# Kernel optimization log

Measured on AMD Instinct MI355X. Metric: run time of the kernel, lower is better.

Reference implementation:

```python
import jax, jax.numpy as jnp
import numpy as np

IMG = 128
FX, FY, CX, CY = 588.03, 587.07, 320.0, 240.0
FLIP = 1.0
SAMPLE = 1024  # sample_num in Img2pcl
N_VERTS = 778


def setup_inputs() -> dict:
    key = jax.random.key(0)
    ks = jax.random.split(key, 6)
    B = 64
    real = jax.random.uniform(ks[0], (B, 1, IMG, IMG), jnp.float32)   # normalized depth in [0,1)
    synth = jax.random.uniform(ks[1], (B, 1, IMG, IMG), jnp.float32)  # unused by forward
    verts = jax.random.normal(ks[2], (B, N_VERTS, 3), jnp.float32)
    faces = jax.random.randint(ks[3], (1538, 3), 0, N_VERTS, jnp.int32)  # unused by forward
    center = jax.random.normal(ks[4], (B, 3), jnp.float32) * 0.1 + jnp.array([0.0, 0.0, 400.0], jnp.float32)
    # crop matrix must be invertible: identity plus small perturbation
    M = jnp.eye(3, dtype=jnp.float32)[None] + 0.1 * jax.random.normal(ks[5], (B, 3, 3), jnp.float32)
    cube = jnp.full((B, 3), 250.0, jnp.float32)
    return dict(real=real, synth=synth, verts=verts, faces=faces, center=center, M=M, cube=cube)


def _img2pcl(real, center, M, cube):
    """Vectorized Img2pcl: normalized (u,v,d) -> normalized xyz for every pixel, plus valid mask."""
    B = real.shape[0]
    # input already IMG x IMG so F.interpolate is identity
    img = real[:, 0]                                   # [B,H,W]
    t = 2.0 * jnp.arange(IMG, dtype=jnp.float32) / (IMG - 1.0) - 1.0
    mesh_x = jnp.broadcast_to(t[:, None], (IMG, IMG))  # varies along rows (v)
    mesh_y = jnp.broadcast_to(t[None, :], (IMG, IMG))  # varies along cols (u)
    uvd = jnp.stack([
        jnp.broadcast_to(mesh_y, (B, IMG, IMG)),
        jnp.broadcast_to(mesh_x, (B, IMG, IMG)),
        img,
    ], axis=-1).reshape(B, IMG * IMG, 3)               # [B,P,3]
    # unnormalize uv and depth
    uv = (uvd[..., :2] + 1.0) * (IMG / 2.0)
    d = uvd[..., 2] * (cube[:, None, 2] / 2.0) + center[:, None, 2]   # [B,P]
    # get_trans_points with M^{-1}
    M_inv = jnp.linalg.inv(M)                          # [B,3,3]
    h = jnp.concatenate([uv, jnp.ones_like(uv[..., :1])], axis=-1)    # [B,P,3]
    uv_w = jnp.einsum('bij,bpj->bpi', M_inv, h)[..., :2]
    # pointsImgTo3D (pinhole back-projection)
    x = (uv_w[..., 0] - CX) * d / FX
    y = FLIP * (uv_w[..., 1] - CY) * d / FY
    xyz = jnp.stack([x, y, d], axis=-1)                # [B,P,3]
    xyz_n = (xyz - center[:, None, :]) / (cube[:, None, :] / 2.0)
    mask = img.reshape(B, -1) <= 0.99                  # valid (foreground) pixels
    return xyz_n, mask


def reference(real, synth, verts, faces, center, M, cube):
    xyz, mask = _img2pcl(real, center, M, cube)
    # torch.multinomial(uniform weights, SAMPLE, without replacement) over valid pixels
    # == Gumbel top-k over the masked candidate set (jit-compatible, fixed shapes)
    u = jax.random.uniform(jax.random.key(1), mask.shape)
    gumbel = -jnp.log(-jnp.log(u + 1e-20) + 1e-20)
    score = jnp.where(mask, gumbel, -jnp.inf)
    _, idx = jax.lax.top_k(score, SAMPLE)              # [B,SAMPLE]
    pcl1 = jnp.take_along_axis(xyz, idx[..., None], axis=1)  # [B,SAMPLE,3]
    # chamfer distance (pytorch3d-style: mean-reduced squared-dist NN, both directions)
    d2 = jnp.sum((pcl1[:, :, None, :] - verts[:, None, :, :]) ** 2, axis=-1)  # [B,SAMPLE,V]
    loss = d2.min(axis=2).mean() + d2.min(axis=1).mean()
    return loss
```

## Files before the change

### kernel.cpp

```cpp
#include <hip/hip_runtime.h>
#include <stdint.h>
#include <math.h>

#define NPIX   16384
#define SAMPLE 1024
#define NV     778
#define BATCH  64

#define A_SCALE (1.0f / (float)(BATCH * SAMPLE))
#define B_SCALE (1.0f / (float)(BATCH * NV))

__device__ __forceinline__ uint32_t rotl32(uint32_t v, int r) {
  return (v << r) | (v >> (32 - r));
}

__device__ __forceinline__ uint32_t threefry_bits(uint32_t g) {
  uint32_t ks0 = 0u, ks1 = 1u;
  uint32_t ks2 = ks0 ^ ks1 ^ 0x1BD11BDAu;
  uint32_t x0 = 0u + ks0, x1 = g + ks1;
#define TF_R(r) { x0 += x1; x1 = rotl32(x1, (r)); x1 ^= x0; }
  TF_R(13) TF_R(15) TF_R(26) TF_R(6)
  x0 += ks1; x1 += ks2 + 1u;
  TF_R(17) TF_R(29) TF_R(16) TF_R(24)
  x0 += ks2; x1 += ks0 + 2u;
  TF_R(13) TF_R(15) TF_R(26) TF_R(6)
  x0 += ks0; x1 += ks1 + 3u;
  TF_R(17) TF_R(29) TF_R(16) TF_R(24)
  x0 += ks1; x1 += ks2 + 4u;
  TF_R(13) TF_R(15) TF_R(26) TF_R(6)
  x0 += ks2; x1 += ks0 + 5u;
#undef TF_R
  return x0 ^ x1;
}

__device__ __forceinline__ float waveReduceSum(float v) {
#pragma unroll
  for (int off = 32; off > 0; off >>= 1) v += __shfl_down(v, off, 64);
  return v;
}

__global__ __launch_bounds__(1024) void select_kernel(
    const float4* __restrict__ real4,
    const float* __restrict__ center,
    const float* __restrict__ M,
    const float* __restrict__ cube,
    float4* __restrict__ pcl4,
    float* __restrict__ out) {
  const int b = blockIdx.x;
  const int tid = threadIdx.x;
  const int lane = tid & 63;
  const int wv = tid >> 6;

  if (b == 0 && tid == 0) out[0] = 0.0f;

  __shared__ uint32_t hist[512];
  __shared__ uint32_t wt[8], offs[8];
  __shared__ uint64_t cand[512];
  __shared__ float candrv[512];
  __shared__ float sh_minv[6], sh_c[3], sh_hb[3];
  __shared__ uint32_t sh_cnt, sh_ccnt, sh_bstar, sh_above;

  if (tid == 0) {
    const float* m = M + (size_t)b * 9;
    float m00=m[0], m01=m[1], m02=m[2];
    float m10=m[3], m11=m[4], m12=m[5];
    float m20=m[6], m21=m[7], m22=m[8];
    float c00 = m11*m22 - m12*m21;
    float c10 = m12*m20 - m10*m22;
    float c20 = m10*m21 - m11*m20;
    float det = m00*c00 + m01*c10 + m02*c20;
    float id = 1.0f / det;
    sh_minv[0] = c00 * id;
    sh_minv[1] = (m02*m21 - m01*m22) * id;
    sh_minv[2] = (m01*m12 - m02*m11) * id;
    sh_minv[3] = c10 * id;
    sh_minv[4] = (m00*m22 - m02*m20) * id;
    sh_minv[5] = (m02*m10 - m00*m12) * id;
    sh_c[0] = center[b*3+0]; sh_c[1] = center[b*3+1]; sh_c[2] = center[b*3+2];
    sh_hb[0] = cube[b*3+0]*0.5f; sh_hb[1] = cube[b*3+1]*0.5f; sh_hb[2] = cube[b*3+2]*0.5f;
    sh_cnt = 0; sh_ccnt = 0;
  }
  if (tid < 512) hist[tid] = 0;

  uint32_t uv[16];
  float    rv[16];
  const float4* rb4 = real4 + (size_t)b * (NPIX / 4);
#pragma unroll
  for (int e4 = 0; e4 < 4; ++e4) {
    float4 im = rb4[e4 * 1024 + tid];
    uint32_t base = (uint32_t)(b * NPIX + e4 * 4096) + (uint32_t)(tid << 2);
    rv[e4*4+0] = im.x; rv[e4*4+1] = im.y; rv[e4*4+2] = im.z; rv[e4*4+3] = im.w;
    uv[e4*4+0] = (im.x <= 0.99f) ? ((threefry_bits(base + 0u) >> 9) + 1u) : 0u;
    uv[e4*4+1] = (im.y <= 0.99f) ? ((threefry_bits(base + 1u) >> 9) + 1u) : 0u;
    uv[e4*4+2] = (im.z <= 0.99f) ? ((threefry_bits(base + 2u) >> 9) + 1u) : 0u;
    uv[e4*4+3] = (im.w <= 0.99f) ? ((threefry_bits(base + 3u) >> 9) + 1u) : 0u;
  }
  __syncthreads();

#pragma unroll
  for (int e = 0; e < 16; ++e)
    if (uv[e]) atomicAdd(&hist[(uv[e] - 1u) >> 14], 1u);
  __syncthreads();

  uint32_t cnt = 0, sfx = 0;
  if (tid < 512) {
    cnt = hist[tid];
    sfx = cnt;
#pragma unroll
    for (int off = 1; off < 64; off <<= 1) {
      uint32_t u = __shfl_down(sfx, off, 64);
      if (lane + off < 64) sfx += u;
    }
    if (lane == 0) wt[wv] = sfx;
  }
  __syncthreads();
  if (tid < 8) {
    uint32_t t = wt[tid], s = t;
#pragma unroll
    for (int off = 1; off < 8; off <<= 1) {
      uint32_t u = __shfl_down(s, off, 64);
      if (tid + off < 8) s += u;
    }
    offs[tid] = s - t;
  }
  __syncthreads();
  if (tid < 512) {
    uint32_t tot = sfx + offs[wv];
    uint32_t above = tot - cnt;
    if (tot >= SAMPLE && above < SAMPLE && cnt > 0) {
      sh_bstar = (uint32_t)tid;
      sh_above = above;
    }
  }
  __syncthreads();
  const int bstar = (int)sh_bstar;
  const uint32_t kneed = SAMPLE - sh_above;

  float4* ob = pcl4 + (size_t)b * SAMPLE;
  auto emit = [&](int p, float depth01, uint32_t slot) {
    int i = p >> 7, j = p & 127;
    float tj = (2.0f * (float)j) / 127.0f - 1.0f;
    float ti = (2.0f * (float)i) / 127.0f - 1.0f;
    float u0 = (tj + 1.0f) * 64.0f;
    float u1 = (ti + 1.0f) * 64.0f;
    float d  = depth01 * sh_hb[2] + sh_c[2];
    float w0 = sh_minv[0]*u0 + sh_minv[1]*u1 + sh_minv[2];
    float w1 = sh_minv[3]*u0 + sh_minv[4]*u1 + sh_minv[5];
    float x = (w0 - 320.0f) * d / 588.03f;
    float y = (w1 - 240.0f) * d / 587.07f;
    float4 o;
    o.x = (x - sh_c[0]) / sh_hb[0];
    o.y = (y - sh_c[1]) / sh_hb[1];
    o.z = (d - sh_c[2]) / sh_hb[2];
    o.w = 0.0f;
    ob[slot] = o;
  };

#pragma unroll
  for (int e = 0; e < 16; ++e) {
    uint32_t v = uv[e];
    int p = (e >> 2) * 4096 + (tid << 2) + (e & 3);
    int bk = v ? (int)((v - 1u) >> 14) : -1;
    bool hi = (bk > bstar);
    unsigned long long m = __ballot(hi);
    if (m) {
      int leader = __ffsll((unsigned long long)m) - 1;
      uint32_t base;
      if (lane == leader) base = atomicAdd(&sh_cnt, (uint32_t)__popcll(m));
      base = __shfl(base, leader, 64);
      if (hi) emit(p, rv[e], base + (uint32_t)__popcll(m & ((1ull << lane) - 1ull)));
    }
    bool eqb = (bk == bstar);
    unsigned long long m2 = __ballot(eqb);
    if (m2) {
      int leader = __ffsll((unsigned long long)m2) - 1;
      uint32_t cb;
      if (lane == leader) cb = atomicAdd(&sh_ccnt, (uint32_t)__popcll(m2));
      cb = __shfl(cb, leader, 64);
      if (eqb) {
        uint32_t ci = cb + (uint32_t)__popcll(m2 & ((1ull << lane) - 1ull));
        if (ci < 512) {
          cand[ci] = ((uint64_t)v << 14) | (uint64_t)(16383 - p);
          candrv[ci] = rv[e];
        }
      }
    }
  }
  __syncthreads();

  uint32_t c = sh_ccnt; if (c > 512) c = 512;
  if (tid < 64) {
    for (uint32_t basei = 0; basei < c; basei += 64) {
      uint32_t i = basei + (uint32_t)lane;
      bool act = (i < c);
      uint64_t ki = act ? cand[i] : 0ull;
      uint32_t rank = 0;
      for (uint32_t j2 = 0; j2 < c; ++j2) rank += (cand[j2] > ki) ? 1u : 0u;
      bool sel = act && (rank < kneed);
      unsigned long long m = __ballot(sel);
      if (m) {
        int leader = __ffsll((unsigned long long)m) - 1;
        uint32_t base;
        if (lane == leader) base = atomicAdd(&sh_cnt, (uint32_t)__popcll(m));
        base = __shfl(base, leader, 64);
        if (sel) {
          int p = 16383 - (int)(ki & 0x3FFFull);
          emit(p, candrv[i], base + (uint32_t)__popcll(m & ((1ull << lane) - 1ull)));
        }
      }
    }
  }
}

#define NA_BLOCKS 512
#define NB_SLICES 7
#define NB_BLOCKS (BATCH * NB_SLICES)

__global__ __launch_bounds__(256, 4) void dist_kernel(
    const float* __restrict__ verts,
    const float4* __restrict__ pcl4,
    float* __restrict__ out) {
  __shared__ __align__(16) uint8_t shbuf[20992];
  __shared__ float red[4];
  const int blk = blockIdx.x;
  const int tid = threadIdx.x;
  const int s = tid >> 5;
  const int g = tid & 31;
  float val = 0.0f;

  if (blk < NA_BLOCKS) {
    const int b = blk >> 3, slice = blk & 7;
    float4* sv4 = (float4*)shbuf;
    float* pmin = (float*)(shbuf + 12448);
    float* npl  = (float*)(shbuf + 16544);
    const float* vb = verts + (size_t)b * NV * 3;
    for (int v = tid; v < NV; v += 256) {
      float x = vb[v*3], y = vb[v*3+1], z = vb[v*3+2];
      float4 t;
      t.x = -2.0f*x; t.y = -2.0f*y; t.z = -2.0f*z; t.w = x*x + y*y + z*z;
      sv4[v] = t;
    }
    const float4* pb = pcl4 + (size_t)b * SAMPLE + slice * 128;
    float px[4], py[4], pz[4], np[4], mn[4];
#pragma unroll
    for (int j = 0; j < 4; ++j) {
      float4 q = pb[j * 32 + g];
      px[j] = q.x; py[j] = q.y; pz[j] = q.z;
      np[j] = q.x*q.x + q.y*q.y + q.z*q.z;
      mn[j] = INFINITY;
    }
    __syncthreads();
    const int vs = s * 98;
    const int ve = (vs + 98 < NV) ? vs + 98 : NV;
    for (int v = vs; v < ve; ++v) {
      float4 vv = sv4[v];
#pragma unroll
      for (int j = 0; j < 4; ++j) {
        float t = fmaf(pz[j], vv.z, fmaf(py[j], vv.y, fmaf(px[j], vv.x, vv.w)));
        mn[j] = fminf(mn[j], t);
      }
    }
#pragma unroll
    for (int j = 0; j < 4; ++j) {
      pmin[s * 128 + j * 32 + g] = mn[j];
      if (s == 0) npl[j * 32 + g] = np[j];
    }
    __syncthreads();
    if (tid < 128) {
      float m = pmin[tid];
#pragma unroll
      for (int ss = 1; ss < 8; ++ss) m = fminf(m, pmin[ss * 128 + tid]);
      val = (m + npl[tid]) * A_SCALE;
    }
  } else {
    const int bb = blk - NA_BLOCKS;
    const int b = bb / NB_SLICES, slice = bb % NB_SLICES;
    float4* sp4 = (float4*)shbuf;
    float* vmin = (float*)(shbuf + 16384);
    float* nvl  = (float*)(shbuf + 20480);
    const float4* pcb = pcl4 + (size_t)b * SAMPLE;
    for (int i = tid; i < SAMPLE; i += 256) {
      float4 q = pcb[i];
      float4 t;
      t.x = -2.0f*q.x; t.y = -2.0f*q.y; t.z = -2.0f*q.z;
      t.w = q.x*q.x + q.y*q.y + q.z*q.z;
      sp4[i] = t;
    }
    const float* vb = verts + (size_t)b * NV * 3;
    const int vbase = slice * 128;
    float vx[4], vy[4], vz[4], nv[4], mn[4];
#pragma unroll
    for (int j = 0; j < 4; ++j) {
      int v = vbase + j * 32 + g;
      int vc = (v < NV) ? v : 0;
      vx[j] = vb[vc*3]; vy[j] = vb[vc*3+1]; vz[j] = vb[vc*3+2];
      nv[j] = vx[j]*vx[j] + vy[j]*vy[j] + vz[j]*vz[j];
      mn[j] = INFINITY;
    }
    __syncthreads();
    const int ps = s * 128;
    for (int i = 0; i < 128; ++i) {
      float4 pt = sp4[ps + i];
#pragma unroll
      for (int j = 0; j < 4; ++j) {
        float t = fmaf(vz[j], pt.z, fmaf(vy[j], pt.y, fmaf(vx[j], pt.x, pt.w)));
        mn[j] = fminf(mn[j], t);
      }
    }
#pragma unroll
    for (int j = 0; j < 4; ++j) {
      vmin[s * 128 + j * 32 + g] = mn[j];
      if (s == 0) nvl[j * 32 + g] = nv[j];
    }
    __syncthreads();
    if (tid < 128 && (vbase + tid) < NV) {
      float m = vmin[tid];
#pragma unroll
      for (int ss = 1; ss < 8; ++ss) m = fminf(m, vmin[ss * 128 + tid]);
      val = (m + nvl[tid]) * B_SCALE;
    }
  }

  float r = waveReduceSum(val);
  if ((tid & 63) == 0) red[tid >> 6] = r;
  __syncthreads();
  if (tid == 0) atomicAdd(out, red[0] + red[1] + red[2] + red[3]);
}

extern "C" void kernel_launch(void* const* d_in, const int* in_sizes, int n_in,
                              void* d_out, int out_size, void* d_ws, size_t ws_size,
                              hipStream_t stream) {
  const float* real   = (const float*)d_in[0];
  const float* verts  = (const float*)d_in[2];
  const float* center = (const float*)d_in[4];
  const float* M      = (const float*)d_in[5];
  const float* cube   = (const float*)d_in[6];

  float4* pcl4 = (float4*)d_ws;
  float* out = (float*)d_out;

  select_kernel<<<dim3(BATCH), dim3(1024), 0, stream>>>(
      (const float4*)real, center, M, cube, pcl4, out);
  dist_kernel<<<dim3(NA_BLOCKS + NB_BLOCKS), dim3(256), 0, stream>>>(
      verts, pcl4, out);
}
```

Before: 115.8 us.

## Fuse select and chamfer into one cooperative kernel with four blocks per batch

Replaces the two-launch pipeline (select_kernel with 64 blocks, then dist_kernel) with one cooperative kernel of 256 blocks, four per batch item, synchronised by grid.sync. Each block handles a quarter of the pixels for the histogram radix threshold and emit step. Boundary-bucket candidates go through global memory for a rank-based tie resolution, and each block then computes a quarter of the chamfer distances. This aims to use more CUs in the selection phase and to drop a kernel launch, at the cost of three grid-wide barriers, global atomics and a cooperative-launch requirement with fallback to the old path.

After: 252.6 us. 2.18x slower.

```diff
diff --git a/kernel.cpp b/kernel.cpp
--- a/kernel.cpp
+++ b/kernel.cpp
@@ -1,6 +1,9 @@
 #include <hip/hip_runtime.h>
+#include <hip/hip_cooperative_groups.h>
 #include <stdint.h>
 #include <math.h>
+
+namespace cg = cooperative_groups;
 
 #define NPIX   16384
 #define SAMPLE 1024
@@ -9,6 +12,14 @@
 
 #define A_SCALE (1.0f / (float)(BATCH * SAMPLE))
 #define B_SCALE (1.0f / (float)(BATCH * NV))
+
+#define WS_PCL    0u
+#define WS_HISTP  1048576u
+#define WS_CAND   1572864u
+#define WS_CANDRV 1835008u
+#define WS_CNT    1966080u
+#define WS_CCNT   1966336u
+#define WS_NEEDED 1966592u
 
 __device__ __forceinline__ uint32_t rotl32(uint32_t v, int r) {
   return (v << r) | (v >> (32 - r));
@@ -37,6 +48,291 @@
 #pragma unroll
   for (int off = 32; off > 0; off >>= 1) v += __shfl_down(v, off, 64);
   return v;
+}
+
+__global__ __launch_bounds__(1024) void fused_kernel(
+    const float4* __restrict__ real4,
+    const float* __restrict__ verts,
+    const float* __restrict__ center,
+    const float* __restrict__ M,
+    const float* __restrict__ cube,
+    float* __restrict__ out,
+    float4* __restrict__ pcl4,
+    uint32_t* __restrict__ histp,
+    uint64_t* __restrict__ candg,
+    float* __restrict__ candrvg,
+    uint32_t* __restrict__ cnts,
+    uint32_t* __restrict__ ccnts) {
+  cg::grid_group grid = cg::this_grid();
+  const int bq = blockIdx.x;
+  const int b = bq >> 2, q = bq & 3;
+  const int tid = threadIdx.x;
+  const int lane = tid & 63;
+  const int wv = tid >> 6;
+
+  __shared__ __align__(16) uint8_t shbuf[45216];
+  __shared__ uint32_t wt[8], offs[8];
+  __shared__ float sh_minv[6], sh_c[3], sh_hb[3];
+  __shared__ uint32_t sh_bstar, sh_above;
+  __shared__ float red[16];
+
+  uint32_t* hist = (uint32_t*)shbuf;
+
+  if (bq == 0 && tid == 0) out[0] = 0.0f;
+  if (q == 0 && tid == 0) { cnts[b] = 0u; ccnts[b] = 0u; }
+  if (tid == 0) {
+    const float* m = M + (size_t)b * 9;
+    float m00=m[0], m01=m[1], m02=m[2];
+    float m10=m[3], m11=m[4], m12=m[5];
+    float m20=m[6], m21=m[7], m22=m[8];
+    float c00 = m11*m22 - m12*m21;
+    float c10 = m12*m20 - m10*m22;
+    float c20 = m10*m21 - m11*m20;
+    float det = m00*c00 + m01*c10 + m02*c20;
+    float id = 1.0f / det;
+    sh_minv[0] = c00 * id;
+    sh_minv[1] = (m02*m21 - m01*m22) * id;
+    sh_minv[2] = (m01*m12 - m02*m11) * id;
+    sh_minv[3] = c10 * id;
+    sh_minv[4] = (m00*m22 - m02*m20) * id;
+    sh_minv[5] = (m02*m10 - m00*m12) * id;
+    sh_c[0] = center[b*3+0]; sh_c[1] = center[b*3+1]; sh_c[2] = center[b*3+2];
+    sh_hb[0] = cube[b*3+0]*0.5f; sh_hb[1] = cube[b*3+1]*0.5f; sh_hb[2] = cube[b*3+2]*0.5f;
+  }
+  if (tid < 512) hist[tid] = 0u;
+
+  float4 im = real4[(size_t)b * 4096 + q * 1024 + tid];
+  uint32_t base = (uint32_t)(b * NPIX + q * 4096) + (uint32_t)(tid << 2);
+  uint32_t uvr[4]; float rvr[4];
+  rvr[0] = im.x; rvr[1] = im.y; rvr[2] = im.z; rvr[3] = im.w;
+  uvr[0] = (im.x <= 0.99f) ? ((threefry_bits(base + 0u) >> 9) + 1u) : 0u;
+  uvr[1] = (im.y <= 0.99f) ? ((threefry_bits(base + 1u) >> 9) + 1u) : 0u;
+  uvr[2] = (im.z <= 0.99f) ? ((threefry_bits(base + 2u) >> 9) + 1u) : 0u;
+  uvr[3] = (im.w <= 0.99f) ? ((threefry_bits(base + 3u) >> 9) + 1u) : 0u;
+  __syncthreads();
+#pragma unroll
+  for (int c = 0; c < 4; ++c)
+    if (uvr[c]) atomicAdd(&hist[(uvr[c] - 1u) >> 14], 1u);
+  __syncthreads();
+  if (tid < 512) histp[(size_t)bq * 512 + tid] = hist[tid];
+
+  grid.sync();
+
+  uint32_t cnt = 0, sfx = 0;
+  if (tid < 512) {
+    const uint32_t* hp = histp + (size_t)(b << 2) * 512 + tid;
+    cnt = hp[0] + hp[512] + hp[1024] + hp[1536];
+    sfx = cnt;
+#pragma unroll
+    for (int off = 1; off < 64; off <<= 1) {
+      uint32_t u = __shfl_down(sfx, off, 64);
+      if (lane + off < 64) sfx += u;
+    }
+    if (lane == 0) wt[wv] = sfx;
+  }
+  __syncthreads();
+  if (tid < 8) {
+    uint32_t t = wt[tid], s = t;
+#pragma unroll
+    for (int off = 1; off < 8; off <<= 1) {
+      uint32_t u = __shfl_down(s, off, 64);
+      if (tid + off < 8) s += u;
+    }
+    offs[tid] = s - t;
+  }
+  __syncthreads();
+  if (tid < 512) {
+    uint32_t tot = sfx + offs[wv];
+    uint32_t above = tot - cnt;
+    if (tot >= SAMPLE && above < SAMPLE && cnt > 0) {
+      sh_bstar = (uint32_t)tid;
+      sh_above = above;
+    }
+  }
+  __syncthreads();
+  const int bstar = (int)sh_bstar;
+  const uint32_t kneed = SAMPLE - sh_above;
+
+  float4* ob = pcl4 + (size_t)b * SAMPLE;
+  auto emit = [&](int p, float depth01, uint32_t slot) {
+    int i = p >> 7, j = p & 127;
+    float tj = (2.0f * (float)j) / 127.0f - 1.0f;
+    float ti = (2.0f * (float)i) / 127.0f - 1.0f;
+    float u0 = (tj + 1.0f) * 64.0f;
+    float u1 = (ti + 1.0f) * 64.0f;
+    float d  = depth01 * sh_hb[2] + sh_c[2];
+    float w0 = sh_minv[0]*u0 + sh_minv[1]*u1 + sh_minv[2];
+    float w1 = sh_minv[3]*u0 + sh_minv[4]*u1 + sh_minv[5];
+    float x = (w0 - 320.0f) * d / 588.03f;
+    float y = (w1 - 240.0f) * d / 587.07f;
+    float4 o;
+    o.x = (x - sh_c[0]) / sh_hb[0];
+    o.y = (y - sh_c[1]) / sh_hb[1];
+    o.z = (d - sh_c[2]) / sh_hb[2];
+    o.w = 0.0f;
+    ob[slot] = o;
+  };
+
+  uint64_t* cb_ = candg + (size_t)b * 512;
+  float*    crv_ = candrvg + (size_t)b * 512;
+#pragma unroll
+  for (int c = 0; c < 4; ++c) {
+    uint32_t v = uvr[c];
+    int p = q * 4096 + (tid << 2) + c;
+    int bk = v ? (int)((v - 1u) >> 14) : -1;
+    bool hi = (bk > bstar);
+    unsigned long long m = __ballot(hi);
+    if (m) {
+      int leader = __ffsll((unsigned long long)m) - 1;
+      uint32_t bslot;
+      if (lane == leader) bslot = atomicAdd(&cnts[b], (uint32_t)__popcll(m));
+      bslot = __shfl(bslot, leader, 64);
+      if (hi) emit(p, rvr[c], bslot + (uint32_t)__popcll(m & ((1ull << lane) - 1ull)));
+    }
+    bool eqb = (bk == bstar);
+    unsigned long long m2 = __ballot(eqb);
+    if (m2) {
+      int leader = __ffsll((unsigned long long)m2) - 1;
+      uint32_t cb;
+      if (lane == leader) cb = atomicAdd(&ccnts[b], (uint32_t)__popcll(m2));
+      cb = __shfl(cb, leader, 64);
+      if (eqb) {
+        uint32_t ci = cb + (uint32_t)__popcll(m2 & ((1ull << lane) - 1ull));
+        if (ci < 512) {
+          cb_[ci] = ((uint64_t)v << 14) | (uint64_t)(16383 - p);
+          crv_[ci] = rvr[c];
+        }
+      }
+    }
+  }
+
+  grid.sync();
+
+  if (q == 0) {
+    uint32_t c = ccnts[b]; if (c > 512u) c = 512u;
+    if (tid < 64) {
+      for (uint32_t basei = 0; basei < c; basei += 64) {
+        uint32_t i = basei + (uint32_t)lane;
+        bool act = (i < c);
+        uint64_t ki = act ? cb_[i] : 0ull;
+        uint32_t rank = 0;
+        for (uint32_t j2 = 0; j2 < c; ++j2) rank += (cb_[j2] > ki) ? 1u : 0u;
+        bool sel = act && (rank < kneed);
+        unsigned long long m = __ballot(sel);
+        if (m) {
+          int leader = __ffsll((unsigned long long)m) - 1;
+          uint32_t bslot;
+          if (lane == leader) bslot = atomicAdd(&cnts[b], (uint32_t)__popcll(m));
+          bslot = __shfl(bslot, leader, 64);
+          if (sel) {
+            int p = 16383 - (int)(ki & 0x3FFFull);
+            emit(p, crv_[i], bslot + (uint32_t)__popcll(m & ((1ull << lane) - 1ull)));
+          }
+        }
+      }
+    }
+  }
+
+  grid.sync();
+
+  float4* sv4 = (float4*)shbuf;
+  float4* sp4 = (float4*)(shbuf + 12448);
+  float*  fbuf = (float*)(shbuf + 28832);
+
+  const float* vb = verts + (size_t)b * NV * 3;
+  if (tid < NV) {
+    float x = vb[tid*3], y = vb[tid*3+1], z = vb[tid*3+2];
+    float4 t;
+    t.x = -2.0f*x; t.y = -2.0f*y; t.z = -2.0f*z; t.w = x*x + y*y + z*z;
+    sv4[tid] = t;
+  }
+  {
+    float4 qd = ob[tid];
+    float4 t;
+    t.x = -2.0f*qd.x; t.y = -2.0f*qd.y; t.z = -2.0f*qd.z;
+    t.w = qd.x*qd.x + qd.y*qd.y + qd.z*qd.z;
+    sp4[tid] = t;
+  }
+  __syncthreads();
+
+  float val = 0.0f;
+  const int sub = tid & 63;
+  const int seg16 = tid >> 6;
+
+  {
+    float px[4], py[4], pz[4], mnA[4];
+#pragma unroll
+    for (int j = 0; j < 4; ++j) {
+      float4 sp = sp4[q * 256 + j * 64 + sub];
+      px[j] = -0.5f * sp.x; py[j] = -0.5f * sp.y; pz[j] = -0.5f * sp.z;
+      mnA[j] = INFINITY;
+    }
+    int vs = seg16 * 49, ve = vs + 49; if (ve > NV) ve = NV;
+    for (int v = vs; v < ve; ++v) {
+      float4 vv = sv4[v];
+#pragma unroll
+      for (int j = 0; j < 4; ++j) {
+        float t = fmaf(pz[j], vv.z, fmaf(py[j], vv.y, fmaf(px[j], vv.x, vv.w)));
+        mnA[j] = fminf(mnA[j], t);
+      }
+    }
+#pragma unroll
+    for (int j = 0; j < 4; ++j) fbuf[seg16 * 256 + j * 64 + sub] = mnA[j];
+  }
+  __syncthreads();
+  if (tid < 256) {
+    float m = fbuf[tid];
+#pragma unroll
+    for (int s2 = 1; s2 < 16; ++s2) m = fminf(m, fbuf[s2 * 256 + tid]);
+    val += (m + sp4[q * 256 + tid].w) * A_SCALE;
+  }
+  __syncthreads();
+
+  {
+    const int vbase = q * 195;
+    int nsl = NV - vbase; if (nsl > 195) nsl = 195;
+    float vx[4], vy[4], vz[4], mnB[4];
+#pragma unroll
+    for (int j = 0; j < 4; ++j) {
+      int vloc = j * 64 + sub;
+      int vi = (vloc < nsl) ? (vbase + vloc) : 0;
+      float4 sv = sv4[vi];
+      vx[j] = -0.5f * sv.x; vy[j] = -0.5f * sv.y; vz[j] = -0.5f * sv.z;
+      mnB[j] = INFINITY;
+    }
+    int is = seg16 * 64;
+    for (int i = 0; i < 64; ++i) {
+      float4 pp = sp4[is + i];
+#pragma unroll
+      for (int j = 0; j < 4; ++j) {
+        float t = fmaf(vz[j], pp.z, fmaf(vy[j], pp.y, fmaf(vx[j], pp.x, pp.w)));
+        mnB[j] = fminf(mnB[j], t);
+      }
+    }
+#pragma unroll
+    for (int j = 0; j < 4; ++j) fbuf[seg16 * 256 + j * 64 + sub] = mnB[j];
+  }
+  __syncthreads();
+  {
+    const int vbase = q * 195;
+    int nsl = NV - vbase; if (nsl > 195) nsl = 195;
+    if (tid < nsl) {
+      float m = fbuf[tid];
+#pragma unroll
+      for (int s2 = 1; s2 < 16; ++s2) m = fminf(m, fbuf[s2 * 256 + tid]);
+      val += (m + sv4[vbase + tid].w) * B_SCALE;
+    }
+  }
+
+  float r = waveReduceSum(val);
+  if (lane == 0) red[wv] = r;
+  __syncthreads();
+  if (tid == 0) {
+    float s = 0.0f;
+#pragma unroll
+    for (int i = 0; i < 16; ++i) s += red[i];
+    atomicAdd(out, s);
+  }
 }
 
 __global__ __launch_bounds__(1024) void select_kernel(
@@ -335,9 +631,37 @@
   const float* center = (const float*)d_in[4];
   const float* M      = (const float*)d_in[5];
   const float* cube   = (const float*)d_in[6];
-
-  float4* pcl4 = (float4*)d_ws;
   float* out = (float*)d_out;
+
+  uint8_t* w = (uint8_t*)d_ws;
+  float4*   pcl4    = (float4*)(w + WS_PCL);
+  uint32_t* histp   = (uint32_t*)(w + WS_HISTP);
+  uint64_t* candg   = (uint64_t*)(w + WS_CAND);
+  float*    candrvg = (float*)(w + WS_CANDRV);
+  uint32_t* cnts    = (uint32_t*)(w + WS_CNT);
+  uint32_t* ccnts   = (uint32_t*)(w + WS_CCNT);
+
+  static int coop = -1;
+  if (coop < 0) {
+    int dev = 0, v = 0;
+    (void)hipGetDevice(&dev);
+    if (hipDeviceGetAttribute(&v, hipDeviceAttributeCooperativeLaunch, dev) != hipSuccess) v = 0;
+    coop = v ? 1 : 0;
+  }
+
+  if (coop == 1 && ws_size >= (size_t)WS_NEEDED) {
+    const float4* real4 = (const float4*)real;
+    void* args[] = {
+      (void*)&real4, (void*)&verts, (void*)&center, (void*)&M, (void*)&cube,
+      (void*)&out, (void*)&pcl4, (void*)&histp, (void*)&candg, (void*)&candrvg,
+      (void*)&cnts, (void*)&ccnts
+    };
+    hipError_t e = hipLaunchCooperativeKernel(
+        reinterpret_cast<void*>(fused_kernel), dim3(BATCH * 4), dim3(1024),
+        args, 0, stream);
+    if (e == hipSuccess) return;
+    (void)hipGetLastError();
+  }
 
   select_kernel<<<dim3(BATCH), dim3(1024), 0, stream>>>(
       (const float4*)real, center, M, cube, pcl4, out);
```

## Fuse selection and chamfer distance into one kernel with redundant per-quarter selection

Applied to the files above, without the earlier changes.

Merges the sampling/selection kernel and the distance kernel into a single launch of 256 blocks, four per batch. Each block redoes the full top-k selection for its batch and keeps the selected points in shared memory, then computes one quarter of each chamfer direction. Atomic-based compaction is replaced with deterministic block-wide prefix scans, and the output is zeroed with a memset. This removes the global workspace round trip and the second launch, at the cost of repeating the threefry hashing and selection four times per batch and using large shared memory with 1024-thread blocks.

Result: faster. 109.9 us (-5.2%).

```diff
diff --git a/kernel.cpp b/kernel.cpp
--- a/kernel.cpp
+++ b/kernel.cpp
@@ -39,26 +39,60 @@
   return v;
 }
 
-__global__ __launch_bounds__(1024) void select_kernel(
+__device__ __forceinline__ uint32_t blockExclScan1024(
+    uint32_t v, volatile uint32_t* swt, volatile uint32_t* soffs,
+    uint32_t* total) {
+  const int tid = threadIdx.x;
+  const int lane = tid & 63;
+  const int wv = tid >> 6;
+  __syncthreads();
+  uint32_t incl = v;
+#pragma unroll
+  for (int off = 1; off < 64; off <<= 1) {
+    uint32_t u = __shfl_up(incl, off, 64);
+    if (lane >= off) incl += u;
+  }
+  if (lane == 63) swt[wv] = incl;
+  __syncthreads();
+  if (tid < 16) {
+    uint32_t t = swt[tid], s = t;
+#pragma unroll
+    for (int off = 1; off < 16; off <<= 1) {
+      uint32_t u = __shfl_up(s, off, 64);
+      if (lane >= off) s += u;
+    }
+    soffs[tid] = s - t;
+  }
+  __syncthreads();
+  *total = soffs[15] + swt[15];
+  return soffs[wv] + incl - v;
+}
+
+__global__ __launch_bounds__(1024) void mega_kernel(
     const float4* __restrict__ real4,
+    const float* __restrict__ verts,
     const float* __restrict__ center,
     const float* __restrict__ M,
     const float* __restrict__ cube,
-    float4* __restrict__ pcl4,
     float* __restrict__ out) {
-  const int b = blockIdx.x;
+  const int bq = blockIdx.x;
+  const int b = bq >> 2, q = bq & 3;
   const int tid = threadIdx.x;
   const int lane = tid & 63;
   const int wv = tid >> 6;
 
-  if (b == 0 && tid == 0) out[0] = 0.0f;
-
-  __shared__ uint32_t hist[512];
+  __shared__ __align__(16) uint8_t shbuf[53408];
+  float4*   sv4    = (float4*)shbuf;
+  float4*   sp4    = (float4*)(shbuf + 12448);
+  float*    fbuf   = (float*)(shbuf + 28832);
+  uint32_t* hist   = (uint32_t*)(shbuf + 45216);
+  uint64_t* cand   = (uint64_t*)(shbuf + 47264);
+  float*    candrv = (float*)(shbuf + 51360);
   __shared__ uint32_t wt[8], offs[8];
-  __shared__ uint64_t cand[512];
-  __shared__ float candrv[512];
+  __shared__ uint32_t swt[16], soffs[16];
   __shared__ float sh_minv[6], sh_c[3], sh_hb[3];
-  __shared__ uint32_t sh_cnt, sh_ccnt, sh_bstar, sh_above;
+  __shared__ uint32_t sh_bstar, sh_above;
+  __shared__ float red[16];
 
   if (tid == 0) {
     const float* m = M + (size_t)b * 9;
@@ -78,18 +112,25 @@
     sh_minv[5] = (m02*m10 - m00*m12) * id;
     sh_c[0] = center[b*3+0]; sh_c[1] = center[b*3+1]; sh_c[2] = center[b*3+2];
     sh_hb[0] = cube[b*3+0]*0.5f; sh_hb[1] = cube[b*3+1]*0.5f; sh_hb[2] = cube[b*3+2]*0.5f;
-    sh_cnt = 0; sh_ccnt = 0;
-  }
-  if (tid < 512) hist[tid] = 0;
+  }
+  if (tid < 512) hist[tid] = 0u;
+
+  const float* vb = verts + (size_t)b * NV * 3;
+  for (int v = tid; v < NV; v += 1024) {
+    float x = vb[v*3], y = vb[v*3+1], z = vb[v*3+2];
+    float4 t;
+    t.x = -2.0f*x; t.y = -2.0f*y; t.z = -2.0f*z; t.w = x*x + y*y + z*z;
+    sv4[v] = t;
+  }
 
   uint32_t uv[16];
-  float    rv[16];
+  float    rvv[16];
   const float4* rb4 = real4 + (size_t)b * (NPIX / 4);
 #pragma unroll
   for (int e4 = 0; e4 < 4; ++e4) {
     float4 im = rb4[e4 * 1024 + tid];
     uint32_t base = (uint32_t)(b * NPIX + e4 * 4096) + (uint32_t)(tid << 2);
-    rv[e4*4+0] = im.x; rv[e4*4+1] = im.y; rv[e4*4+2] = im.z; rv[e4*4+3] = im.w;
+    rvv[e4*4+0] = im.x; rvv[e4*4+1] = im.y; rvv[e4*4+2] = im.z; rvv[e4*4+3] = im.w;
     uv[e4*4+0] = (im.x <= 0.99f) ? ((threefry_bits(base + 0u) >> 9) + 1u) : 0u;
     uv[e4*4+1] = (im.y <= 0.99f) ? ((threefry_bits(base + 1u) >> 9) + 1u) : 0u;
     uv[e4*4+2] = (im.z <= 0.99f) ? ((threefry_bits(base + 2u) >> 9) + 1u) : 0u;
@@ -134,9 +175,9 @@
   }
   __syncthreads();
   const int bstar = (int)sh_bstar;
-  const uint32_t kneed = SAMPLE - sh_above;
-
-  float4* ob = pcl4 + (size_t)b * SAMPLE;
+  const uint32_t above = sh_above;
+  const uint32_t kneed = SAMPLE - above;
+
   auto emit = [&](int p, float depth01, uint32_t slot) {
     int i = p >> 7, j = p & 127;
     float tj = (2.0f * (float)j) / 127.0f - 1.0f;
@@ -148,183 +189,140 @@
     float w1 = sh_minv[3]*u0 + sh_minv[4]*u1 + sh_minv[5];
     float x = (w0 - 320.0f) * d / 588.03f;
     float y = (w1 - 240.0f) * d / 587.07f;
-    float4 o;
-    o.x = (x - sh_c[0]) / sh_hb[0];
-    o.y = (y - sh_c[1]) / sh_hb[1];
-    o.z = (d - sh_c[2]) / sh_hb[2];
-    o.w = 0.0f;
-    ob[slot] = o;
+    float ox = (x - sh_c[0]) / sh_hb[0];
+    float oy = (y - sh_c[1]) / sh_hb[1];
+    float oz = (d - sh_c[2]) / sh_hb[2];
+    float4 t;
+    t.x = -2.0f*ox; t.y = -2.0f*oy; t.z = -2.0f*oz;
+    t.w = ox*ox + oy*oy + oz*oz;
+    sp4[slot] = t;
   };
 
+  uint32_t ch = 0, ce = 0;
 #pragma unroll
   for (int e = 0; e < 16; ++e) {
-    uint32_t v = uv[e];
-    int p = (e >> 2) * 4096 + (tid << 2) + (e & 3);
-    int bk = v ? (int)((v - 1u) >> 14) : -1;
-    bool hi = (bk > bstar);
-    unsigned long long m = __ballot(hi);
-    if (m) {
-      int leader = __ffsll((unsigned long long)m) - 1;
-      uint32_t base;
-      if (lane == leader) base = atomicAdd(&sh_cnt, (uint32_t)__popcll(m));
-      base = __shfl(base, leader, 64);
-      if (hi) emit(p, rv[e], base + (uint32_t)__popcll(m & ((1ull << lane) - 1ull)));
-    }
-    bool eqb = (bk == bstar);
-    unsigned long long m2 = __ballot(eqb);
-    if (m2) {
-      int leader = __ffsll((unsigned long long)m2) - 1;
-      uint32_t cb;
-      if (lane == leader) cb = atomicAdd(&sh_ccnt, (uint32_t)__popcll(m2));
-      cb = __shfl(cb, leader, 64);
-      if (eqb) {
-        uint32_t ci = cb + (uint32_t)__popcll(m2 & ((1ull << lane) - 1ull));
-        if (ci < 512) {
-          cand[ci] = ((uint64_t)v << 14) | (uint64_t)(16383 - p);
-          candrv[ci] = rv[e];
+    int bk = uv[e] ? (int)((uv[e] - 1u) >> 14) : -1;
+    ch += (bk > bstar) ? 1u : 0u;
+    ce += (bk == bstar) ? 1u : 0u;
+  }
+  uint32_t htot, etot;
+  uint32_t hoff = blockExclScan1024(ch, swt, soffs, &htot);
+  uint32_t eoff = blockExclScan1024(ce, swt, soffs, &etot);
+
+  {
+    uint32_t h = hoff, eo = eoff;
+#pragma unroll
+    for (int e = 0; e < 16; ++e) {
+      uint32_t v = uv[e];
+      int bk = v ? (int)((v - 1u) >> 14) : -1;
+      int p = (e >> 2) * 4096 + (tid << 2) + (e & 3);
+      if (bk > bstar) {
+        emit(p, rvv[e], h++);
+      } else if (bk == bstar) {
+        if (eo < 512u) {
+          cand[eo] = ((uint64_t)v << 14) | (uint64_t)(16383 - p);
+          candrv[eo] = rvv[e];
         }
+        eo++;
       }
     }
   }
   __syncthreads();
 
-  uint32_t c = sh_ccnt; if (c > 512) c = 512;
-  if (tid < 64) {
-    for (uint32_t basei = 0; basei < c; basei += 64) {
-      uint32_t i = basei + (uint32_t)lane;
-      bool act = (i < c);
-      uint64_t ki = act ? cand[i] : 0ull;
-      uint32_t rank = 0;
-      for (uint32_t j2 = 0; j2 < c; ++j2) rank += (cand[j2] > ki) ? 1u : 0u;
-      bool sel = act && (rank < kneed);
-      unsigned long long m = __ballot(sel);
-      if (m) {
-        int leader = __ffsll((unsigned long long)m) - 1;
-        uint32_t base;
-        if (lane == leader) base = atomicAdd(&sh_cnt, (uint32_t)__popcll(m));
-        base = __shfl(base, leader, 64);
-        if (sel) {
-          int p = 16383 - (int)(ki & 0x3FFFull);
-          emit(p, candrv[i], base + (uint32_t)__popcll(m & ((1ull << lane) - 1ull)));
-        }
-      }
-    }
-  }
-}
-
-#define NA_BLOCKS 512
-#define NB_SLICES 7
-#define NB_BLOCKS (BATCH * NB_SLICES)
-
-__global__ __launch_bounds__(256, 4) void dist_kernel(
-    const float* __restrict__ verts,
-    const float4* __restrict__ pcl4,
-    float* __restrict__ out) {
-  __shared__ __align__(16) uint8_t shbuf[20992];
-  __shared__ float red[4];
-  const int blk = blockIdx.x;
-  const int tid = threadIdx.x;
-  const int s = tid >> 5;
-  const int g = tid & 31;
+  uint32_t c = etot; if (c > 512u) c = 512u;
+  uint32_t selbit = 0; uint64_t ki = 0;
+  if (tid < (int)c) {
+    ki = cand[tid];
+    uint32_t rank = 0;
+    for (uint32_t j2 = 0; j2 < c; ++j2) rank += (cand[j2] > ki) ? 1u : 0u;
+    selbit = (rank < kneed) ? 1u : 0u;
+  }
+  uint32_t stot;
+  uint32_t soff2 = blockExclScan1024(selbit, swt, soffs, &stot);
+  if (selbit) {
+    int p = 16383 - (int)(ki & 0x3FFFull);
+    emit(p, candrv[tid], above + soff2);
+  }
+  __syncthreads();
+
   float val = 0.0f;
-
-  if (blk < NA_BLOCKS) {
-    const int b = blk >> 3, slice = blk & 7;
-    float4* sv4 = (float4*)shbuf;
-    float* pmin = (float*)(shbuf + 12448);
-    float* npl  = (float*)(shbuf + 16544);
-    const float* vb = verts + (size_t)b * NV * 3;
-    for (int v = tid; v < NV; v += 256) {
-      float x = vb[v*3], y = vb[v*3+1], z = vb[v*3+2];
-      float4 t;
-      t.x = -2.0f*x; t.y = -2.0f*y; t.z = -2.0f*z; t.w = x*x + y*y + z*z;
-      sv4[v] = t;
-    }
-    const float4* pb = pcl4 + (size_t)b * SAMPLE + slice * 128;
-    float px[4], py[4], pz[4], np[4], mn[4];
+  const int sub = tid & 63;
+  const int seg16 = tid >> 6;
+
+  {
+    float px[4], py[4], pz[4], mnA[4];
 #pragma unroll
     for (int j = 0; j < 4; ++j) {
-      float4 q = pb[j * 32 + g];
-      px[j] = q.x; py[j] = q.y; pz[j] = q.z;
-      np[j] = q.x*q.x + q.y*q.y + q.z*q.z;
-      mn[j] = INFINITY;
-    }
-    __syncthreads();
-    const int vs = s * 98;
-    const int ve = (vs + 98 < NV) ? vs + 98 : NV;
+      float4 sp = sp4[q * 256 + j * 64 + sub];
+      px[j] = -0.5f * sp.x; py[j] = -0.5f * sp.y; pz[j] = -0.5f * sp.z;
+      mnA[j] = INFINITY;
+    }
+    int vs = seg16 * 49, ve = vs + 49; if (ve > NV) ve = NV;
     for (int v = vs; v < ve; ++v) {
       float4 vv = sv4[v];
 #pragma unroll
       for (int j = 0; j < 4; ++j) {
         float t = fmaf(pz[j], vv.z, fmaf(py[j], vv.y, fmaf(px[j], vv.x, vv.w)));
-        mn[j] = fminf(mn[j], t);
+        mnA[j] = fminf(mnA[j], t);
       }
     }
 #pragma unroll
+    for (int j = 0; j < 4; ++j) fbuf[seg16 * 256 + j * 64 + sub] = mnA[j];
+  }
+  __syncthreads();
+  if (tid < 256) {
+    float m = fbuf[tid];
+#pragma unroll
+    for (int s2 = 1; s2 < 16; ++s2) m = fminf(m, fbuf[s2 * 256 + tid]);
+    val += (m + sp4[q * 256 + tid].w) * A_SCALE;
+  }
+  __syncthreads();
+
+  {
+    const int vbase = q * 195;
+    int nsl = NV - vbase; if (nsl > 195) nsl = 195;
+    float vx[4], vy[4], vz[4], mnB[4];
+#pragma unroll
     for (int j = 0; j < 4; ++j) {
-      pmin[s * 128 + j * 32 + g] = mn[j];
-      if (s == 0) npl[j * 32 + g] = np[j];
-    }
-    __syncthreads();
-    if (tid < 128) {
-      float m = pmin[tid];
-#pragma unroll
-      for (int ss = 1; ss < 8; ++ss) m = fminf(m, pmin[ss * 128 + tid]);
-      val = (m + npl[tid]) * A_SCALE;
-    }
-  } else {
-    const int bb = blk - NA_BLOCKS;
-    const int b = bb / NB_SLICES, slice = bb % NB_SLICES;
-    float4* sp4 = (float4*)shbuf;
-    float* vmin = (float*)(shbuf + 16384);
-    float* nvl  = (float*)(shbuf + 20480);
-    const float4* pcb = pcl4 + (size_t)b * SAMPLE;
-    for (int i = tid; i < SAMPLE; i += 256) {
-      float4 q = pcb[i];
-      float4 t;
-      t.x = -2.0f*q.x; t.y = -2.0f*q.y; t.z = -2.0f*q.z;
-      t.w = q.x*q.x + q.y*q.y + q.z*q.z;
-      sp4[i] = t;
-    }
-    const float* vb = verts + (size_t)b * NV * 3;
-    const int vbase = slice * 128;
-    float vx[4], vy[4], vz[4], nv[4], mn[4];
-#pragma unroll
-    for (int j = 0; j < 4; ++j) {
-      int v = vbase + j * 32 + g;
-      int vc = (v < NV) ? v : 0;
-      vx[j] = vb[vc*3]; vy[j] = vb[vc*3+1]; vz[j] = vb[vc*3+2];
-      nv[j] = vx[j]*vx[j] + vy[j]*vy[j] + vz[j]*vz[j];
-      mn[j] = INFINITY;
-    }
-    __syncthreads();
-    const int ps = s * 128;
-    for (int i = 0; i < 128; ++i) {
-      float4 pt = sp4[ps + i];
+      int vloc = j * 64 + sub;
+      int vi = (vloc < nsl) ? (vbase + vloc) : 0;
+      float4 sv = sv4[vi];
+      vx[j] = -0.5f * sv.x; vy[j] = -0.5f * sv.y; vz[j] = -0.5f * sv.z;
+      mnB[j] = INFINITY;
+    }
+    int is = seg16 * 64;
+    for (int i = 0; i < 64; ++i) {
+      float4 pp = sp4[is + i];
 #pragma unroll
       for (int j = 0; j < 4; ++j) {
-        float t = fmaf(vz[j], pt.z, fmaf(vy[j], pt.y, fmaf(vx[j], pt.x, pt.w)));
-        mn[j] = fminf(mn[j], t);
+        float t = fmaf(vz[j], pp.z, fmaf(vy[j], pp.y, fmaf(vx[j], pp.x, pp.w)));
+        mnB[j] = fminf(mnB[j], t);
       }
     }
 #pragma unroll
-    for (int j = 0; j < 4; ++j) {
-      vmin[s * 128 + j * 32 + g] = mn[j];
-      if (s == 0) nvl[j * 32 + g] = nv[j];
-    }
-    __syncthreads();
-    if (tid < 128 && (vbase + tid) < NV) {
-      float m = vmin[tid];
-#pragma unroll
-      for (int ss = 1; ss < 8; ++ss) m = fminf(m, vmin[ss * 128 + tid]);
-      val = (m + nvl[tid]) * B_SCALE;
+    for (int j = 0; j < 4; ++j) fbuf[seg16 * 256 + j * 64 + sub] = mnB[j];
+  }
+  __syncthreads();
+  {
+    const int vbase = q * 195;
+    int nsl = NV - vbase; if (nsl > 195) nsl = 195;
+    if (tid < nsl) {
+      float m = fbuf[tid];
+#pragma unroll
+      for (int s2 = 1; s2 < 16; ++s2) m = fminf(m, fbuf[s2 * 256 + tid]);
+      val += (m + sv4[vbase + tid].w) * B_SCALE;
     }
   }
 
   float r = waveReduceSum(val);
-  if ((tid & 63) == 0) red[tid >> 6] = r;
-  __syncthreads();
-  if (tid == 0) atomicAdd(out, red[0] + red[1] + red[2] + red[3]);
+  if (lane == 0) red[wv] = r;
+  __syncthreads();
+  if (tid == 0) {
+    float s = 0.0f;
+#pragma unroll
+    for (int i = 0; i < 16; ++i) s += red[i];
+    atomicAdd(out, s);
+  }
 }
 
 extern "C" void kernel_launch(void* const* d_in, const int* in_sizes, int n_in,
@@ -335,12 +333,9 @@
   const float* center = (const float*)d_in[4];
   const float* M      = (const float*)d_in[5];
   const float* cube   = (const float*)d_in[6];
-
-  float4* pcl4 = (float4*)d_ws;
   float* out = (float*)d_out;
 
-  select_kernel<<<dim3(BATCH), dim3(1024), 0, stream>>>(
-      (const float4*)real, center, M, cube, pcl4, out);
-  dist_kernel<<<dim3(NA_BLOCKS + NB_BLOCKS), dim3(256), 0, stream>>>(
-      verts, pcl4, out);
-}
+  hipMemsetAsync(out, 0, sizeof(float), stream);
+  mega_kernel<<<dim3(BATCH * 4), dim3(1024), 0, stream>>>(
+      (const float4*)real, verts, center, M, cube, out);
+}
```
